# Kernel optimization log

Hardware: AMD Instinct MI355X
Metric: run time of the kernel (lower is better)

## Reference

```python
import jax, jax.numpy as jnp
import numpy as np

N_INST = 131072      # total patches across all bags
D_EMB = 512          # VGG16 pooling='max' output dim
ATT_UNITS = 128
CLS_UNITS = 512
NUM_BAGS = 256


def setup_inputs() -> dict:
    key = jax.random.key(0)
    ks = jax.random.split(key, 16)
    first_emb = jax.random.normal(ks[0], (N_INST, D_EMB), dtype=jnp.float32)
    first_lab = jnp.sort(jax.random.randint(ks[1], (N_INST,), 0, NUM_BAGS)).astype(jnp.int64)
    s = 0.02
    return {
        "first_emb": first_emb,
        "first_lab": first_lab,
        # first-level attention head: Dense(tanh) -> Dense(1, sigmoid)
        "W_a1": jax.random.normal(ks[2], (D_EMB, ATT_UNITS), dtype=jnp.float32) * s,
        "b_a1": jnp.zeros((ATT_UNITS,), dtype=jnp.float32),
        "w_o1": jax.random.normal(ks[3], (ATT_UNITS, 1), dtype=jnp.float32) * s,
        "b_o1": jnp.zeros((1,), dtype=jnp.float32),
        # second-level attention head
        "W_a2": jax.random.normal(ks[4], (D_EMB, ATT_UNITS), dtype=jnp.float32) * s,
        "b_a2": jnp.zeros((ATT_UNITS,), dtype=jnp.float32),
        "w_o2": jax.random.normal(ks[5], (ATT_UNITS, 1), dtype=jnp.float32) * s,
        "b_o2": jnp.zeros((1,), dtype=jnp.float32),
        # classifier: Dense(CLS_UNITS, linear) -> Dense(1, sigmoid)
        "W_c": jax.random.normal(ks[6], (D_EMB, CLS_UNITS), dtype=jnp.float32) * s,
        "b_c": jnp.zeros((CLS_UNITS,), dtype=jnp.float32),
        "w_out": jax.random.normal(ks[7], (CLS_UNITS, 1), dtype=jnp.float32) * s,
        "b_out": jnp.zeros((1,), dtype=jnp.float32),
    }


def reference(first_emb, first_lab, W_a1, b_a1, w_o1, b_o1,
              W_a2, b_a2, w_o2, b_o2, W_c, b_c, w_out, b_out):
    # --- first-level (instance) attention ---
    a1 = jnp.tanh(first_emb @ W_a1 + b_a1)                 # [N, A]
    att1 = jax.nn.sigmoid(a1 @ w_o1 + b_o1)                # [N, 1]
    # tf: transpose(softmax(transpose(att))) == softmax over the N axis (global)
    fst_att = jax.nn.softmax(att1, axis=0)                 # [N, 1]
    # --- per-bag attention-weighted sum (fused segment reduce) ---
    # replaces the python loop of gather_nd + matmul over contiguous bags
    second_emb = jax.ops.segment_sum(fst_att * first_emb, first_lab,
                                     num_segments=NUM_BAGS)  # [B, D]
    # --- second-level (bag) attention ---
    a2 = jnp.tanh(second_emb @ W_a2 + b_a2)                # [B, A]
    att2 = jax.nn.sigmoid(a2 @ w_o2 + b_o2)                # [B, 1]
    snd_att = jax.nn.softmax(att2.T, axis=-1)              # [1, B]
    outer_bag_emb = snd_att @ second_emb                   # [1, D]
    # --- classifier (dropout is identity at inference) ---
    h = outer_bag_emb @ W_c + b_c                          # [1, CLS]
    pred = jax.nn.sigmoid(h @ w_out + b_out)               # [1, 1]
    return pred
```

## Files before the change

kernel.cpp:

```cpp
#include <hip/hip_runtime.h>
#include <cstdint>
#include <cstddef>

#define N_INST 131072
#define D_EMB  512
#define ATT    128
#define NBAGS  256
#define TILE_I 64
#define LDA    520

typedef __attribute__((ext_vector_type(8))) short  bf16x8;
typedef __attribute__((ext_vector_type(4))) float  f32x4;
typedef __attribute__((ext_vector_type(4))) unsigned short u16x4;


__device__ inline unsigned short f2b(float f) {
    unsigned u = __builtin_bit_cast(unsigned, f);
    u += 0x7FFFu + ((u >> 16) & 1u);
    return (unsigned short)(u >> 16);
}

__device__ inline float fast_tanh(float x) {
    float e = __expf(2.f * x);
    return 1.f - 2.f / (e + 1.f);
}

__global__ __launch_bounds__(256) void k_prep_wt(
    const float* __restrict__ Wa1, unsigned short* __restrict__ Wt)
{
    const int n = blockIdx.x;
    for (int k = threadIdx.x; k < D_EMB; k += 256)
        Wt[(size_t)n * D_EMB + k] = f2b(Wa1[(size_t)k * ATT + n]);
}

__global__ __launch_bounds__(256, 2) void k_att1(
    const float* __restrict__ emb, const int* __restrict__ lab,
    const unsigned short* __restrict__ Wt, const float* __restrict__ ba1,
    const float* __restrict__ wo1, const float* __restrict__ bo1,
    float* __restrict__ rawr, int R, float* __restrict__ Z1)
{
    __shared__ unsigned short Ash[TILE_I * LDA];
    __shared__ float att4[4][TILE_I];
    __shared__ float sval[TILE_I];
    __shared__ int   labs[TILE_I];

    const int t  = threadIdx.x;
    const int w  = t >> 6;
    const int l  = t & 63;
    const int l4 = l & 15;
    const int h4 = l >> 4;
    const size_t i0 = (size_t)blockIdx.x * TILE_I;
    float* __restrict__ raw = rawr + (size_t)(blockIdx.x % R) * (NBAGS * D_EMB);

    if (t < TILE_I) labs[t] = lab[i0 + t];

    bf16x8 bfrag[2][16];
    #pragma unroll
    for (int nt = 0; nt < 2; ++nt) {
        const int n = 16 * (2 * w + nt) + l4;
        #pragma unroll
        for (int ks = 0; ks < 16; ++ks)
            bfrag[nt][ks] = *reinterpret_cast<const bf16x8*>(
                &Wt[(size_t)n * D_EMB + 32 * ks + 8 * h4]);
    }

    float ba1v[2], wo1v[2];
    #pragma unroll
    for (int nt = 0; nt < 2; ++nt) {
        int c = 16 * (2 * w + nt) + l4;
        ba1v[nt] = ba1[c];
        wo1v[nt] = wo1[c];
    }

    #pragma unroll
    for (int g = 0; g < 2; ++g) {
        float4 v[16];
        #pragma unroll
        for (int j = 0; j < 16; ++j) {
            int idx = (g * 16 + j) * 256 + t;
            int row = idx >> 7;
            int c4  = (idx & 127) * 4;
            v[j] = *reinterpret_cast<const float4*>(&emb[(i0 + row) * D_EMB + c4]);
        }
        #pragma unroll
        for (int j = 0; j < 16; ++j) {
            int idx = (g * 16 + j) * 256 + t;
            int row = idx >> 7;
            int c4  = (idx & 127) * 4;
            u16x4 b = { f2b(v[j].x), f2b(v[j].y), f2b(v[j].z), f2b(v[j].w) };
            *reinterpret_cast<u16x4*>(&Ash[row * LDA + c4]) = b;
        }
    }
    __syncthreads();

    f32x4 acc[4][2];
    #pragma unroll
    for (int rt = 0; rt < 4; ++rt) {
        acc[rt][0] = (f32x4){0.f, 0.f, 0.f, 0.f};
        acc[rt][1] = (f32x4){0.f, 0.f, 0.f, 0.f};
    }
    #pragma unroll
    for (int rt = 0; rt < 4; ++rt) {
        #pragma unroll
        for (int ks = 0; ks < 16; ++ks) {
            bf16x8 af = *reinterpret_cast<const bf16x8*>(
                &Ash[(16 * rt + l4) * LDA + 32 * ks + 8 * h4]);
            acc[rt][0] = __builtin_amdgcn_mfma_f32_16x16x32_bf16(
                af, bfrag[0][ks], acc[rt][0], 0, 0, 0);
            acc[rt][1] = __builtin_amdgcn_mfma_f32_16x16x32_bf16(
                af, bfrag[1][ks], acc[rt][1], 0, 0, 0);
        }
    }

    #pragma unroll
    for (int rt = 0; rt < 4; ++rt) {
        #pragma unroll
        for (int reg = 0; reg < 4; ++reg) {
            float p = fast_tanh(acc[rt][0][reg] + ba1v[0]) * wo1v[0]
                    + fast_tanh(acc[rt][1][reg] + ba1v[1]) * wo1v[1];
            p += __shfl_xor(p, 1);
            p += __shfl_xor(p, 2);
            p += __shfl_xor(p, 4);
            p += __shfl_xor(p, 8);
            if (l4 == 0) att4[w][16 * rt + 4 * h4 + reg] = p;
        }
    }
    __syncthreads();
    if (t < TILE_I) {
        float a  = att4[0][t] + att4[1][t] + att4[2][t] + att4[3][t] + bo1[0];
        float sg = 1.f / (1.f + __expf(-a));
        sval[t]  = __expf(sg);
    }
    __syncthreads();
    if (t < TILE_I) {
        float z = sval[t];
        #pragma unroll
        for (int m = 1; m < 64; m <<= 1) z += __shfl_xor(z, m);
        if (t == 0) atomicAdd(Z1, z);
    }

    int s0 = 0;
    while (s0 < TILE_I) {
        int bag = labs[s0];
        int s1 = s0 + 1;
        while (s1 < TILE_I && labs[s1] == bag) ++s1;
        float a0 = 0.f, a1 = 0.f;
        #pragma unroll 8
        for (int ii = s0; ii < s1; ++ii) {
            unsigned u = *reinterpret_cast<const unsigned*>(
                &Ash[(size_t)ii * LDA + 2 * t]);
            float lo = __builtin_bit_cast(float, u << 16);
            float hi = __builtin_bit_cast(float, u & 0xffff0000u);
            float s  = sval[ii];
            a0 = fmaf(s, lo, a0);
            a1 = fmaf(s, hi, a1);
        }
        atomicAdd(&raw[bag * D_EMB + 2 * t], a0);
        atomicAdd(&raw[bag * D_EMB + 2 * t + 1], a1);
        s0 = s1;
    }
}

__global__ __launch_bounds__(128) void k_att2(
    const float* __restrict__ Wa2, const float* __restrict__ ba2,
    const float* __restrict__ wo2, const float* __restrict__ bo2,
    float* __restrict__ rawr, int R, const float* __restrict__ Z1,
    float* __restrict__ e2, float* __restrict__ Z2)
{
    __shared__ float sec[D_EMB];
    __shared__ float hh[2];
    const int b = blockIdx.x;
    const int t = threadIdx.x;
    const float zinv = 1.f / Z1[0];
    for (int d = t; d < D_EMB; d += 128) {
        float s = 0.f;
        for (int r = 0; r < R; ++r)
            s += rawr[(size_t)r * (NBAGS * D_EMB) + b * D_EMB + d];
        float v = s * zinv;
        rawr[b * D_EMB + d] = v;
        sec[d] = v;
    }
    __syncthreads();
    float dot = 0.f;
    #pragma unroll 8
    for (int d = 0; d < D_EMB; ++d) dot = fmaf(sec[d], Wa2[d * ATT + t], dot);
    float h = fast_tanh(dot + ba2[t]) * wo2[t];
    #pragma unroll
    for (int m = 1; m < 64; m <<= 1) h += __shfl_xor(h, m);
    if ((t & 63) == 0) hh[t >> 6] = h;
    __syncthreads();
    if (t == 0) {
        float a  = hh[0] + hh[1] + bo2[0];
        float sg = 1.f / (1.f + __expf(-a));
        float e  = __expf(sg);
        e2[b] = e;
        atomicAdd(Z2, e);
    }
}

__global__ __launch_bounds__(256) void k_v(
    const float* __restrict__ Wc, const float* __restrict__ wout,
    float* __restrict__ v)
{
    const int t   = threadIdx.x;
    const int row = blockIdx.x * 8 + (t >> 5);
    const int l   = t & 31;
    float s = 0.f;
    #pragma unroll 4
    for (int c = l; c < 512; c += 32) s = fmaf(Wc[(size_t)row * 512 + c], wout[c], s);
    #pragma unroll
    for (int m = 1; m < 32; m <<= 1) s += __shfl_xor(s, m);
    if (l == 0) v[row] = s;
}

__global__ __launch_bounds__(256) void k_pool(
    const float* __restrict__ raw, const float* __restrict__ e2,
    float* __restrict__ outer)
{
    const int t  = threadIdx.x;
    const int b0 = blockIdx.x * 32;
    float o0 = 0.f, o1 = 0.f;
    for (int b = b0; b < b0 + 32; ++b) {
        float wgt = e2[b];
        float2 r = *reinterpret_cast<const float2*>(&raw[b * D_EMB + 2 * t]);
        o0 = fmaf(wgt, r.x, o0);
        o1 = fmaf(wgt, r.y, o1);
    }
    atomicAdd(&outer[2 * t], o0);
    atomicAdd(&outer[2 * t + 1], o1);
}

__global__ __launch_bounds__(256) void k_cls(
    const float* __restrict__ outer, const float* __restrict__ Z2,
    const float* __restrict__ v, const float* __restrict__ bc,
    const float* __restrict__ wout, const float* __restrict__ bout,
    float* __restrict__ out)
{
    __shared__ float pp[4];
    const int t = threadIdx.x;
    const float z2inv = 1.f / Z2[0];
    float p = (outer[2 * t] * v[2 * t] + outer[2 * t + 1] * v[2 * t + 1]) * z2inv
            + bc[2 * t] * wout[2 * t] + bc[2 * t + 1] * wout[2 * t + 1];
    #pragma unroll
    for (int m = 1; m < 64; m <<= 1) p += __shfl_xor(p, m);
    if ((t & 63) == 0) pp[t >> 6] = p;
    __syncthreads();
    if (t == 0) {
        float s = pp[0] + pp[1] + pp[2] + pp[3] + bout[0];
        out[0] = 1.f / (1.f + __expf(-s));
    }
}

extern "C" void kernel_launch(void* const* d_in, const int* in_sizes, int n_in,
                              void* d_out, int out_size, void* d_ws, size_t ws_size,
                              hipStream_t stream)
{
    const float* emb  = (const float*)d_in[0];
    const int*   lab  = (const int*)d_in[1];
    const float* Wa1  = (const float*)d_in[2];
    const float* ba1  = (const float*)d_in[3];
    const float* wo1  = (const float*)d_in[4];
    const float* bo1  = (const float*)d_in[5];
    const float* Wa2  = (const float*)d_in[6];
    const float* ba2  = (const float*)d_in[7];
    const float* wo2  = (const float*)d_in[8];
    const float* bo2  = (const float*)d_in[9];
    const float* Wc   = (const float*)d_in[10];
    const float* bc   = (const float*)d_in[11];
    const float* wout = (const float*)d_in[12];
    const float* bout = (const float*)d_in[13];

    float* ws    = (float*)d_ws;
    float* Z1    = ws + 0;
    float* Z2    = ws + 1;
    float* v     = ws + 16;
    float* e2    = ws + 1024;
    float* outer = ws + 1536;
    unsigned short* Wt = (unsigned short*)(ws + 4096);
    float* rawr  = ws + 36864;

    const size_t need8 = ((size_t)36864 + 8u * NBAGS * D_EMB) * sizeof(float);
    const int R = (ws_size >= need8) ? 8 : 1;

    hipMemsetAsync(d_ws, 0, ((size_t)36864 + (size_t)R * NBAGS * D_EMB) * sizeof(float), stream);

    hipLaunchKernelGGL(k_prep_wt, dim3(ATT),             dim3(256), 0, stream, Wa1, Wt);
    hipLaunchKernelGGL(k_v,       dim3(64),              dim3(256), 0, stream, Wc, wout, v);
    hipLaunchKernelGGL(k_att1,    dim3(N_INST / TILE_I), dim3(256), 0, stream,
                       emb, lab, Wt, ba1, wo1, bo1, rawr, R, Z1);
    hipLaunchKernelGGL(k_att2,    dim3(NBAGS),           dim3(128), 0, stream,
                       Wa2, ba2, wo2, bo2, rawr, R, Z1, e2, Z2);
    hipLaunchKernelGGL(k_pool,    dim3(8),               dim3(256), 0, stream,
                       rawr, e2, outer);
    hipLaunchKernelGGL(k_cls,     dim3(1),               dim3(256), 0, stream,
                       outer, Z2, v, bc, wout, bout, (float*)d_out);
}
```

Baseline: 141.2 us.

## Split attention-score and segment-sum kernels, double-buffer K chunks in score GEMM

The fused attention kernel becomes two kernels. k_score streams the embedding tile in four 128-wide K chunks through two small LDS buffers, loading the next chunk and its weight fragments while MFMAs run on the current one. The smaller LDS footprint allows 3 blocks per CU, and the per-instance scores go to a global buffer. k_seg then re-reads the fp32 embeddings from global memory to form the per-bag weighted sums. This adds a second full pass over the large embedding matrix and an extra launch in exchange for better overlap and occupancy in the GEMM stage.

```diff
diff --git a/kernel.cpp b/kernel.cpp
--- a/kernel.cpp
+++ b/kernel.cpp
@@ -7,7 +7,8 @@
 #define ATT    128
 #define NBAGS  256
 #define TILE_I 64
-#define LDA    520
+#define KC     128
+#define LDAc   136
 
 typedef __attribute__((ext_vector_type(8))) short  bf16x8;
 typedef __attribute__((ext_vector_type(4))) float  f32x4;
@@ -33,16 +34,14 @@
         Wt[(size_t)n * D_EMB + k] = f2b(Wa1[(size_t)k * ATT + n]);
 }
 
-__global__ __launch_bounds__(256, 2) void k_att1(
-    const float* __restrict__ emb, const int* __restrict__ lab,
+__global__ __launch_bounds__(256, 3) void k_score(
+    const float* __restrict__ emb,
     const unsigned short* __restrict__ Wt, const float* __restrict__ ba1,
     const float* __restrict__ wo1, const float* __restrict__ bo1,
-    float* __restrict__ rawr, int R, float* __restrict__ Z1)
-{
-    __shared__ unsigned short Ash[TILE_I * LDA];
+    float* __restrict__ sval_g, float* __restrict__ Z1)
+{
+    __shared__ unsigned short Ash[2][TILE_I * LDAc];
     __shared__ float att4[4][TILE_I];
-    __shared__ float sval[TILE_I];
-    __shared__ int   labs[TILE_I];
 
     const int t  = threadIdx.x;
     const int w  = t >> 6;
@@ -50,19 +49,6 @@
     const int l4 = l & 15;
     const int h4 = l >> 4;
     const size_t i0 = (size_t)blockIdx.x * TILE_I;
-    float* __restrict__ raw = rawr + (size_t)(blockIdx.x % R) * (NBAGS * D_EMB);
-
-    if (t < TILE_I) labs[t] = lab[i0 + t];
-
-    bf16x8 bfrag[2][16];
-    #pragma unroll
-    for (int nt = 0; nt < 2; ++nt) {
-        const int n = 16 * (2 * w + nt) + l4;
-        #pragma unroll
-        for (int ks = 0; ks < 16; ++ks)
-            bfrag[nt][ks] = *reinterpret_cast<const bf16x8*>(
-                &Wt[(size_t)n * D_EMB + 32 * ks + 8 * h4]);
-    }
 
     float ba1v[2], wo1v[2];
     #pragma unroll
@@ -72,26 +58,37 @@
         wo1v[nt] = wo1[c];
     }
 
-    #pragma unroll
-    for (int g = 0; g < 2; ++g) {
-        float4 v[16];
-        #pragma unroll
-        for (int j = 0; j < 16; ++j) {
-            int idx = (g * 16 + j) * 256 + t;
-            int row = idx >> 7;
-            int c4  = (idx & 127) * 4;
-            v[j] = *reinterpret_cast<const float4*>(&emb[(i0 + row) * D_EMB + c4]);
-        }
-        #pragma unroll
-        for (int j = 0; j < 16; ++j) {
-            int idx = (g * 16 + j) * 256 + t;
-            int row = idx >> 7;
-            int c4  = (idx & 127) * 4;
+    bf16x8 bfA[2][4], bfB[2][4];
+    auto loadB = [&](bf16x8 (&dst)[2][4], int k0) {
+        #pragma unroll
+        for (int nt = 0; nt < 2; ++nt) {
+            const int n = 16 * (2 * w + nt) + l4;
+            #pragma unroll
+            for (int ks = 0; ks < 4; ++ks)
+                dst[nt][ks] = *reinterpret_cast<const bf16x8*>(
+                    &Wt[(size_t)n * D_EMB + k0 + 32 * ks + 8 * h4]);
+        }
+    };
+
+    auto stage = [&](int buf, int k0) {
+        float4 v[8];
+        #pragma unroll
+        for (int j = 0; j < 8; ++j) {
+            int idx = j * 256 + t;
+            int row = idx >> 5;
+            int c4  = (idx & 31) * 4;
+            v[j] = *reinterpret_cast<const float4*>(
+                &emb[(i0 + row) * D_EMB + k0 + c4]);
+        }
+        #pragma unroll
+        for (int j = 0; j < 8; ++j) {
+            int idx = j * 256 + t;
+            int row = idx >> 5;
+            int c4  = (idx & 31) * 4;
             u16x4 b = { f2b(v[j].x), f2b(v[j].y), f2b(v[j].z), f2b(v[j].w) };
-            *reinterpret_cast<u16x4*>(&Ash[row * LDA + c4]) = b;
-        }
-    }
-    __syncthreads();
+            *reinterpret_cast<u16x4*>(&Ash[buf][row * LDAc + c4]) = b;
+        }
+    };
 
     f32x4 acc[4][2];
     #pragma unroll
@@ -99,18 +96,34 @@
         acc[rt][0] = (f32x4){0.f, 0.f, 0.f, 0.f};
         acc[rt][1] = (f32x4){0.f, 0.f, 0.f, 0.f};
     }
-    #pragma unroll
-    for (int rt = 0; rt < 4; ++rt) {
-        #pragma unroll
-        for (int ks = 0; ks < 16; ++ks) {
-            bf16x8 af = *reinterpret_cast<const bf16x8*>(
-                &Ash[(16 * rt + l4) * LDA + 32 * ks + 8 * h4]);
-            acc[rt][0] = __builtin_amdgcn_mfma_f32_16x16x32_bf16(
-                af, bfrag[0][ks], acc[rt][0], 0, 0, 0);
-            acc[rt][1] = __builtin_amdgcn_mfma_f32_16x16x32_bf16(
-                af, bfrag[1][ks], acc[rt][1], 0, 0, 0);
-        }
-    }
+
+    auto mfma_chunk = [&](int buf, bf16x8 (&bfr)[2][4]) {
+        #pragma unroll
+        for (int rt = 0; rt < 4; ++rt) {
+            #pragma unroll
+            for (int ks = 0; ks < 4; ++ks) {
+                bf16x8 af = *reinterpret_cast<const bf16x8*>(
+                    &Ash[buf][(16 * rt + l4) * LDAc + 32 * ks + 8 * h4]);
+                acc[rt][0] = __builtin_amdgcn_mfma_f32_16x16x32_bf16(
+                    af, bfr[0][ks], acc[rt][0], 0, 0, 0);
+                acc[rt][1] = __builtin_amdgcn_mfma_f32_16x16x32_bf16(
+                    af, bfr[1][ks], acc[rt][1], 0, 0, 0);
+            }
+        }
+    };
+
+    stage(0, 0);  loadB(bfA, 0);
+    __syncthreads();
+    stage(1, KC); loadB(bfB, KC);
+    mfma_chunk(0, bfA);
+    __syncthreads();
+    stage(0, 2 * KC); loadB(bfA, 2 * KC);
+    mfma_chunk(1, bfB);
+    __syncthreads();
+    stage(1, 3 * KC); loadB(bfB, 3 * KC);
+    mfma_chunk(0, bfA);
+    __syncthreads();
+    mfma_chunk(1, bfB);
 
     #pragma unroll
     for (int rt = 0; rt < 4; ++rt) {
@@ -129,15 +142,26 @@
     if (t < TILE_I) {
         float a  = att4[0][t] + att4[1][t] + att4[2][t] + att4[3][t] + bo1[0];
         float sg = 1.f / (1.f + __expf(-a));
-        sval[t]  = __expf(sg);
-    }
-    __syncthreads();
-    if (t < TILE_I) {
-        float z = sval[t];
+        float s  = __expf(sg);
+        sval_g[i0 + t] = s;
+        float z = s;
         #pragma unroll
         for (int m = 1; m < 64; m <<= 1) z += __shfl_xor(z, m);
         if (t == 0) atomicAdd(Z1, z);
     }
+}
+
+__global__ __launch_bounds__(256) void k_seg(
+    const float* __restrict__ emb, const int* __restrict__ lab,
+    const float* __restrict__ sval_g, float* __restrict__ rawr, int R)
+{
+    __shared__ float sv[TILE_I];
+    __shared__ int   labs[TILE_I];
+    const int t = threadIdx.x;
+    const size_t i0 = (size_t)blockIdx.x * TILE_I;
+    if (t < TILE_I) { sv[t] = sval_g[i0 + t]; labs[t] = lab[i0 + t]; }
+    __syncthreads();
+    float* __restrict__ raw = rawr + (size_t)(blockIdx.x % R) * (NBAGS * D_EMB);
 
     int s0 = 0;
     while (s0 < TILE_I) {
@@ -145,15 +169,14 @@
         int s1 = s0 + 1;
         while (s1 < TILE_I && labs[s1] == bag) ++s1;
         float a0 = 0.f, a1 = 0.f;
+        const float* ebase = emb + (i0 + s0) * D_EMB + 2 * t;
+        int len = s1 - s0;
         #pragma unroll 8
-        for (int ii = s0; ii < s1; ++ii) {
-            unsigned u = *reinterpret_cast<const unsigned*>(
-                &Ash[(size_t)ii * LDA + 2 * t]);
-            float lo = __builtin_bit_cast(float, u << 16);
-            float hi = __builtin_bit_cast(float, u & 0xffff0000u);
-            float s  = sval[ii];
-            a0 = fmaf(s, lo, a0);
-            a1 = fmaf(s, hi, a1);
+        for (int ii = 0; ii < len; ++ii) {
+            float2 e = *reinterpret_cast<const float2*>(ebase + (size_t)ii * D_EMB);
+            float s = sv[s0 + ii];
+            a0 = fmaf(s, e.x, a0);
+            a1 = fmaf(s, e.y, a1);
         }
         atomicAdd(&raw[bag * D_EMB + 2 * t], a0);
         atomicAdd(&raw[bag * D_EMB + 2 * t + 1], a1);
@@ -270,24 +293,28 @@
     const float* wout = (const float*)d_in[12];
     const float* bout = (const float*)d_in[13];
 
-    float* ws    = (float*)d_ws;
-    float* Z1    = ws + 0;
-    float* Z2    = ws + 1;
-    float* v     = ws + 16;
-    float* e2    = ws + 1024;
-    float* outer = ws + 1536;
+    float* ws     = (float*)d_ws;
+    float* Z1     = ws + 0;
+    float* Z2     = ws + 1;
+    float* v      = ws + 16;
+    float* e2     = ws + 1024;
+    float* outer  = ws + 1536;
     unsigned short* Wt = (unsigned short*)(ws + 4096);
-    float* rawr  = ws + 36864;
-
-    const size_t need8 = ((size_t)36864 + 8u * NBAGS * D_EMB) * sizeof(float);
+    float* rawr   = ws + 36864;
+    float* sval_g = ws + 1085440;
+
+    const size_t need8 = ((size_t)1085440 + N_INST) * sizeof(float);
     const int R = (ws_size >= need8) ? 8 : 1;
+    float* sval = (R == 8) ? sval_g : ws + 36864 + NBAGS * D_EMB;
 
     hipMemsetAsync(d_ws, 0, ((size_t)36864 + (size_t)R * NBAGS * D_EMB) * sizeof(float), stream);
 
     hipLaunchKernelGGL(k_prep_wt, dim3(ATT),             dim3(256), 0, stream, Wa1, Wt);
     hipLaunchKernelGGL(k_v,       dim3(64),              dim3(256), 0, stream, Wc, wout, v);
-    hipLaunchKernelGGL(k_att1,    dim3(N_INST / TILE_I), dim3(256), 0, stream,
-                       emb, lab, Wt, ba1, wo1, bo1, rawr, R, Z1);
+    hipLaunchKernelGGL(k_score,   dim3(N_INST / TILE_I), dim3(256), 0, stream,
+                       emb, Wt, ba1, wo1, bo1, sval, Z1);
+    hipLaunchKernelGGL(k_seg,     dim3(N_INST / TILE_I), dim3(256), 0, stream,
+                       emb, lab, sval, rawr, R);
     hipLaunchKernelGGL(k_att2,    dim3(NBAGS),           dim3(128), 0, stream,
                        Wa2, ba2, wo2, bo2, rawr, R, Z1, e2, Z2);
     hipLaunchKernelGGL(k_pool,    dim3(8),               dim3(256), 0, stream,
```

After: 172.1 us. +21.9%, slower.

## Restructure att1 as per-wave 32-row tiles without shared memory staging

Applied to the files above, without the earlier changes.

Each wavefront now handles 32 instances on its own. It computes all 128 attention columns with MFMA, reading A fragments straight from global memory and B fragments from L2-resident Wt, so the block-wide LDS staging and barriers are gone. The segment sum re-reads embeddings in fp32 and flushes per-bag partials with atomics when the bag changes. The Z1 atomic is spread over 32 slots to reduce contention. The trade-off is that embeddings are read twice from global or cache and Wt is reloaded per tile without register reuse, in exchange for higher occupancy and no LDS traffic.

```diff
diff --git a/kernel.cpp b/kernel.cpp
--- a/kernel.cpp
+++ b/kernel.cpp
@@ -6,12 +6,10 @@
 #define D_EMB  512
 #define ATT    128
 #define NBAGS  256
-#define TILE_I 64
-#define LDA    520
+#define NZ1    32
 
 typedef __attribute__((ext_vector_type(8))) short  bf16x8;
 typedef __attribute__((ext_vector_type(4))) float  f32x4;
-typedef __attribute__((ext_vector_type(4))) unsigned short u16x4;
 
 
 __device__ inline unsigned short f2b(float f) {
@@ -33,145 +31,125 @@
         Wt[(size_t)n * D_EMB + k] = f2b(Wa1[(size_t)k * ATT + n]);
 }
 
-__global__ __launch_bounds__(256, 2) void k_att1(
+__global__ __launch_bounds__(256, 4) void k_att1(
     const float* __restrict__ emb, const int* __restrict__ lab,
     const unsigned short* __restrict__ Wt, const float* __restrict__ ba1,
     const float* __restrict__ wo1, const float* __restrict__ bo1,
-    float* __restrict__ rawr, int R, float* __restrict__ Z1)
-{
-    __shared__ unsigned short Ash[TILE_I * LDA];
-    __shared__ float att4[4][TILE_I];
-    __shared__ float sval[TILE_I];
-    __shared__ int   labs[TILE_I];
-
+    float* __restrict__ rawr, int R, float* __restrict__ Z1s)
+{
     const int t  = threadIdx.x;
     const int w  = t >> 6;
     const int l  = t & 63;
     const int l4 = l & 15;
     const int h4 = l >> 4;
-    const size_t i0 = (size_t)blockIdx.x * TILE_I;
+    const int gw = blockIdx.x * 4 + w;
+    const size_t ib = (size_t)gw * 32;
     float* __restrict__ raw = rawr + (size_t)(blockIdx.x % R) * (NBAGS * D_EMB);
 
-    if (t < TILE_I) labs[t] = lab[i0 + t];
-
-    bf16x8 bfrag[2][16];
-    #pragma unroll
-    for (int nt = 0; nt < 2; ++nt) {
-        const int n = 16 * (2 * w + nt) + l4;
-        #pragma unroll
-        for (int ks = 0; ks < 16; ++ks)
-            bfrag[nt][ks] = *reinterpret_cast<const bf16x8*>(
-                &Wt[(size_t)n * D_EMB + 32 * ks + 8 * h4]);
-    }
-
-    float ba1v[2], wo1v[2];
-    #pragma unroll
-    for (int nt = 0; nt < 2; ++nt) {
-        int c = 16 * (2 * w + nt) + l4;
-        ba1v[nt] = ba1[c];
-        wo1v[nt] = wo1[c];
-    }
-
-    #pragma unroll
-    for (int g = 0; g < 2; ++g) {
-        float4 v[16];
-        #pragma unroll
-        for (int j = 0; j < 16; ++j) {
-            int idx = (g * 16 + j) * 256 + t;
-            int row = idx >> 7;
-            int c4  = (idx & 127) * 4;
-            v[j] = *reinterpret_cast<const float4*>(&emb[(i0 + row) * D_EMB + c4]);
+    const float bo = bo1[0];
+
+    int   cur_bag = -1;
+    float c0 = 0.f, c1 = 0.f, c2 = 0.f, c3 = 0.f;
+    float c4 = 0.f, c5 = 0.f, c6 = 0.f, c7 = 0.f;
+    float z1acc = 0.f;
+
+    #pragma unroll
+    for (int tt = 0; tt < 2; ++tt) {
+        const size_t i0 = ib + tt * 16;
+
+        f32x4 acc[8];
+        #pragma unroll
+        for (int nt = 0; nt < 8; ++nt) acc[nt] = (f32x4){0.f, 0.f, 0.f, 0.f};
+
+        #pragma unroll
+        for (int ks = 0; ks < 16; ++ks) {
+            const float* ap = &emb[(i0 + l4) * D_EMB + 32 * ks + 8 * h4];
+            float4 fa = *reinterpret_cast<const float4*>(ap);
+            float4 fb = *reinterpret_cast<const float4*>(ap + 4);
+            bf16x8 af;
+            af[0] = (short)f2b(fa.x); af[1] = (short)f2b(fa.y);
+            af[2] = (short)f2b(fa.z); af[3] = (short)f2b(fa.w);
+            af[4] = (short)f2b(fb.x); af[5] = (short)f2b(fb.y);
+            af[6] = (short)f2b(fb.z); af[7] = (short)f2b(fb.w);
+            #pragma unroll
+            for (int nt = 0; nt < 8; ++nt) {
+                bf16x8 bf = *reinterpret_cast<const bf16x8*>(
+                    &Wt[(size_t)(l4 + 16 * nt) * D_EMB + 32 * ks + 8 * h4]);
+                acc[nt] = __builtin_amdgcn_mfma_f32_16x16x32_bf16(
+                    af, bf, acc[nt], 0, 0, 0);
+            }
         }
-        #pragma unroll
-        for (int j = 0; j < 16; ++j) {
-            int idx = (g * 16 + j) * 256 + t;
-            int row = idx >> 7;
-            int c4  = (idx & 127) * 4;
-            u16x4 b = { f2b(v[j].x), f2b(v[j].y), f2b(v[j].z), f2b(v[j].w) };
-            *reinterpret_cast<u16x4*>(&Ash[row * LDA + c4]) = b;
-        }
-    }
-    __syncthreads();
-
-    f32x4 acc[4][2];
-    #pragma unroll
-    for (int rt = 0; rt < 4; ++rt) {
-        acc[rt][0] = (f32x4){0.f, 0.f, 0.f, 0.f};
-        acc[rt][1] = (f32x4){0.f, 0.f, 0.f, 0.f};
-    }
-    #pragma unroll
-    for (int rt = 0; rt < 4; ++rt) {
-        #pragma unroll
-        for (int ks = 0; ks < 16; ++ks) {
-            bf16x8 af = *reinterpret_cast<const bf16x8*>(
-                &Ash[(16 * rt + l4) * LDA + 32 * ks + 8 * h4]);
-            acc[rt][0] = __builtin_amdgcn_mfma_f32_16x16x32_bf16(
-                af, bfrag[0][ks], acc[rt][0], 0, 0, 0);
-            acc[rt][1] = __builtin_amdgcn_mfma_f32_16x16x32_bf16(
-                af, bfrag[1][ks], acc[rt][1], 0, 0, 0);
-        }
-    }
-
-    #pragma unroll
-    for (int rt = 0; rt < 4; ++rt) {
+
+        float s4[4];
         #pragma unroll
         for (int reg = 0; reg < 4; ++reg) {
-            float p = fast_tanh(acc[rt][0][reg] + ba1v[0]) * wo1v[0]
-                    + fast_tanh(acc[rt][1][reg] + ba1v[1]) * wo1v[1];
+            float p = 0.f;
+            #pragma unroll
+            for (int nt = 0; nt < 8; ++nt) {
+                int cidx = l4 + 16 * nt;
+                p += fast_tanh(acc[nt][reg] + ba1[cidx]) * wo1[cidx];
+            }
             p += __shfl_xor(p, 1);
             p += __shfl_xor(p, 2);
             p += __shfl_xor(p, 4);
             p += __shfl_xor(p, 8);
-            if (l4 == 0) att4[w][16 * rt + 4 * h4 + reg] = p;
+            float sg = 1.f / (1.f + __expf(-(p + bo)));
+            s4[reg] = __expf(sg);
         }
-    }
-    __syncthreads();
-    if (t < TILE_I) {
-        float a  = att4[0][t] + att4[1][t] + att4[2][t] + att4[3][t] + bo1[0];
-        float sg = 1.f / (1.f + __expf(-a));
-        sval[t]  = __expf(sg);
-    }
-    __syncthreads();
-    if (t < TILE_I) {
-        float z = sval[t];
-        #pragma unroll
-        for (int m = 1; m < 64; m <<= 1) z += __shfl_xor(z, m);
-        if (t == 0) atomicAdd(Z1, z);
-    }
-
-    int s0 = 0;
-    while (s0 < TILE_I) {
-        int bag = labs[s0];
-        int s1 = s0 + 1;
-        while (s1 < TILE_I && labs[s1] == bag) ++s1;
-        float a0 = 0.f, a1 = 0.f;
-        #pragma unroll 8
-        for (int ii = s0; ii < s1; ++ii) {
-            unsigned u = *reinterpret_cast<const unsigned*>(
-                &Ash[(size_t)ii * LDA + 2 * t]);
-            float lo = __builtin_bit_cast(float, u << 16);
-            float hi = __builtin_bit_cast(float, u & 0xffff0000u);
-            float s  = sval[ii];
-            a0 = fmaf(s, lo, a0);
-            a1 = fmaf(s, hi, a1);
+        if (l4 == 0) z1acc += s4[0] + s4[1] + s4[2] + s4[3];
+
+        int lv = lab[i0 + (l & 15)];
+        #pragma unroll
+        for (int r = 0; r < 16; ++r) {
+            int   bag = __shfl(lv, r);
+            float s   = __shfl(s4[r & 3], (r >> 2) * 16);
+            if (bag != cur_bag) {
+                if (cur_bag >= 0) {
+                    float* dst = &raw[cur_bag * D_EMB + 8 * l];
+                    atomicAdd(dst + 0, c0); atomicAdd(dst + 1, c1);
+                    atomicAdd(dst + 2, c2); atomicAdd(dst + 3, c3);
+                    atomicAdd(dst + 4, c4); atomicAdd(dst + 5, c5);
+                    atomicAdd(dst + 6, c6); atomicAdd(dst + 7, c7);
+                }
+                c0 = c1 = c2 = c3 = c4 = c5 = c6 = c7 = 0.f;
+                cur_bag = bag;
+            }
+            const float* ep = &emb[(i0 + r) * D_EMB + 8 * l];
+            float4 e0 = *reinterpret_cast<const float4*>(ep);
+            float4 e1 = *reinterpret_cast<const float4*>(ep + 4);
+            c0 = fmaf(s, e0.x, c0); c1 = fmaf(s, e0.y, c1);
+            c2 = fmaf(s, e0.z, c2); c3 = fmaf(s, e0.w, c3);
+            c4 = fmaf(s, e1.x, c4); c5 = fmaf(s, e1.y, c5);
+            c6 = fmaf(s, e1.z, c6); c7 = fmaf(s, e1.w, c7);
         }
-        atomicAdd(&raw[bag * D_EMB + 2 * t], a0);
-        atomicAdd(&raw[bag * D_EMB + 2 * t + 1], a1);
-        s0 = s1;
-    }
+    }
+
+    if (cur_bag >= 0) {
+        float* dst = &raw[cur_bag * D_EMB + 8 * l];
+        atomicAdd(dst + 0, c0); atomicAdd(dst + 1, c1);
+        atomicAdd(dst + 2, c2); atomicAdd(dst + 3, c3);
+        atomicAdd(dst + 4, c4); atomicAdd(dst + 5, c5);
+        atomicAdd(dst + 6, c6); atomicAdd(dst + 7, c7);
+    }
+    z1acc += __shfl_xor(z1acc, 16);
+    z1acc += __shfl_xor(z1acc, 32);
+    if (l == 0) atomicAdd(&Z1s[gw & (NZ1 - 1)], z1acc);
 }
 
 __global__ __launch_bounds__(128) void k_att2(
     const float* __restrict__ Wa2, const float* __restrict__ ba2,
     const float* __restrict__ wo2, const float* __restrict__ bo2,
-    float* __restrict__ rawr, int R, const float* __restrict__ Z1,
+    float* __restrict__ rawr, int R, const float* __restrict__ Z1s,
     float* __restrict__ e2, float* __restrict__ Z2)
 {
     __shared__ float sec[D_EMB];
     __shared__ float hh[2];
     const int b = blockIdx.x;
     const int t = threadIdx.x;
-    const float zinv = 1.f / Z1[0];
+    float zsum = 0.f;
+    #pragma unroll
+    for (int i = 0; i < NZ1; ++i) zsum += Z1s[i];
+    const float zinv = 1.f / zsum;
     for (int d = t; d < D_EMB; d += 128) {
         float s = 0.f;
         for (int r = 0; r < R; ++r)
@@ -271,9 +249,9 @@
     const float* bout = (const float*)d_in[13];
 
     float* ws    = (float*)d_ws;
-    float* Z1    = ws + 0;
-    float* Z2    = ws + 1;
-    float* v     = ws + 16;
+    float* Z1s   = ws + 0;
+    float* Z2    = ws + 32;
+    float* v     = ws + 64;
     float* e2    = ws + 1024;
     float* outer = ws + 1536;
     unsigned short* Wt = (unsigned short*)(ws + 4096);
@@ -284,14 +262,14 @@
 
     hipMemsetAsync(d_ws, 0, ((size_t)36864 + (size_t)R * NBAGS * D_EMB) * sizeof(float), stream);
 
-    hipLaunchKernelGGL(k_prep_wt, dim3(ATT),             dim3(256), 0, stream, Wa1, Wt);
-    hipLaunchKernelGGL(k_v,       dim3(64),              dim3(256), 0, stream, Wc, wout, v);
-    hipLaunchKernelGGL(k_att1,    dim3(N_INST / TILE_I), dim3(256), 0, stream,
-                       emb, lab, Wt, ba1, wo1, bo1, rawr, R, Z1);
-    hipLaunchKernelGGL(k_att2,    dim3(NBAGS),           dim3(128), 0, stream,
-                       Wa2, ba2, wo2, bo2, rawr, R, Z1, e2, Z2);
-    hipLaunchKernelGGL(k_pool,    dim3(8),               dim3(256), 0, stream,
+    hipLaunchKernelGGL(k_prep_wt, dim3(ATT),   dim3(256), 0, stream, Wa1, Wt);
+    hipLaunchKernelGGL(k_v,       dim3(64),    dim3(256), 0, stream, Wc, wout, v);
+    hipLaunchKernelGGL(k_att1,    dim3(1024),  dim3(256), 0, stream,
+                       emb, lab, Wt, ba1, wo1, bo1, rawr, R, Z1s);
+    hipLaunchKernelGGL(k_att2,    dim3(NBAGS), dim3(128), 0, stream,
+                       Wa2, ba2, wo2, bo2, rawr, R, Z1s, e2, Z2);
+    hipLaunchKernelGGL(k_pool,    dim3(8),     dim3(256), 0, stream,
                        rawr, e2, outer);
-    hipLaunchKernelGGL(k_cls,     dim3(1),               dim3(256), 0, stream,
+    hipLaunchKernelGGL(k_cls,     dim3(1),     dim3(256), 0, stream,
                        outer, Z2, v, bc, wout, bout, (float*)d_out);
 }
```

After: 384.2 us. 172% more time.
